# Kernel optimization log

Measured on AMD Instinct MI355X. Metric: run time of the kernel, lower is better.

## Reference

```python
import jax, jax.numpy as jnp
import numpy as np

B, SQ, SKV = 4, 2048, 2048
DQ, DKV, H, NH = 1024, 1024, 1024, 16
HD = H // NH


def setup_inputs() -> dict:
    key = jax.random.key(0)
    ks = jax.random.split(key, 10)
    s = 0.02
    return {
        "query": jax.random.normal(ks[0], (B, SQ, DQ), jnp.float32),
        "key_value": jax.random.normal(ks[1], (B, SKV, DKV), jnp.float32),
        "Wq": jax.random.normal(ks[2], (DQ, H), jnp.float32) * s,
        "bq": jnp.zeros((H,), jnp.float32),
        "Wk": jax.random.normal(ks[3], (DKV, H), jnp.float32) * s,
        "bk": jnp.zeros((H,), jnp.float32),
        "Wv": jax.random.normal(ks[4], (DKV, H), jnp.float32) * s,
        "bv": jnp.zeros((H,), jnp.float32),
        "Wo": jax.random.normal(ks[5], (H, DQ), jnp.float32) * s,
        "bo": jnp.zeros((DQ,), jnp.float32),
    }


def reference(query, key_value, Wq, bq, Wk, bk, Wv, bv, Wo, bo):
    b, sq, _ = query.shape
    skv = key_value.shape[1]
    scale = np.sqrt(HD).astype(np.float32)
    # project and split heads: [B, S, H] -> [B, NH, S, HD]
    q = (query @ Wq + bq).reshape(b, sq, NH, HD).transpose(0, 2, 1, 3)
    k = (key_value @ Wk + bk).reshape(b, skv, NH, HD).transpose(0, 2, 1, 3)
    v = (key_value @ Wv + bv).reshape(b, skv, NH, HD).transpose(0, 2, 1, 3)
    scores = jnp.einsum("bhqd,bhkd->bhqk", q, k) / scale
    attn = jax.nn.softmax(scores, axis=-1)
    out = jnp.einsum("bhqk,bhkd->bhqd", attn, v)
    out = out.transpose(0, 2, 1, 3).reshape(b, sq, NH * HD)
    return out @ Wo + bo
```

## Files before the change

### kernel.cpp

```cpp
#include <hip/hip_runtime.h>


typedef short s16x8 __attribute__((ext_vector_type(8)));
typedef short s16x4 __attribute__((ext_vector_type(4)));
typedef float f32x4 __attribute__((ext_vector_type(4)));
typedef float f32x16 __attribute__((ext_vector_type(16)));
typedef unsigned short u16;
typedef unsigned int u32;

__device__ __forceinline__ u16 f2bf(float f){
    union{float f;u32 u;} v; v.f=f;
    u32 r = v.u + 0x7fffu + ((v.u>>16)&1u);
    return (u16)(r>>16);
}
__device__ __forceinline__ int swz(int row,int colB){ return row*128 + (colB ^ ((row&7)<<4)); }

__device__ __forceinline__ void gl16(const void* g, void* l){
    __builtin_amdgcn_global_load_lds((__attribute__((address_space(1))) void*)(void*)g,
                                     (__attribute__((address_space(3))) void*)l, 16, 0, 0);
}
__device__ __forceinline__ u32 cvtpk(float lo, float hi){
    u32 r; asm("v_cvt_pk_bf16_f32 %0, %1, %2" : "=v"(r) : "v"(lo), "v"(hi)); return r;
}
__device__ __forceinline__ void plswap(u32& a, u32& b){
    asm("v_permlane32_swap_b32 %0, %1" : "+v"(a), "+v"(b));
}

#define QSCALE 0.1803368801111204f

__global__ __launch_bounds__(256) void cvtbf(const float* __restrict__ in, u16* __restrict__ out){
    size_t i = ((size_t)blockIdx.x*256 + threadIdx.x)*8;
    f32x4 a = *(const f32x4*)(in+i), b = *(const f32x4*)(in+i+4);
    s16x8 o;
    #pragma unroll
    for (int j=0;j<4;++j){ o[j]=(short)f2bf(a[j]); o[4+j]=(short)f2bf(b[j]); }
    *(s16x8*)(out+i) = o;
}

__global__ __launch_bounds__(256) void transW(const float* __restrict__ W, u16* __restrict__ Wt){
    __shared__ u16 T[64*68];
    const int tid = threadIdx.x;
    const int n0 = blockIdx.x*64, k0 = blockIdx.y*64;
    const int tr = tid>>4, tc = (tid&15)*4;
    #pragma unroll
    for (int p=0;p<4;++p){
        int k = p*16 + tr;
        f32x4 v = *(const f32x4*)(W + (size_t)(k0+k)*1024 + n0 + tc);
        s16x4 o;
        #pragma unroll
        for (int j=0;j<4;++j) o[j]=(short)f2bf(v[j]);
        *(s16x4*)(T + k*68 + tc) = o;
    }
    __syncthreads();
    #pragma unroll
    for (int p=0;p<4;++p){
        int n = p*16 + tr;
        s16x4 o;
        #pragma unroll
        for (int e=0;e<4;++e) o[e] = (short)T[(tc+e)*68 + n];
        *(s16x4*)(Wt + (size_t)(n0+n)*1024 + k0 + tc) = o;
    }
}

template<int EPI>
__global__ __launch_bounds__(256)
void gemm128(const u16* __restrict__ A, const u16* __restrict__ Bt,
             const float* __restrict__ bias, void* __restrict__ C,
             int M, int N, int K, float scale)
{
    __shared__ __align__(16) u16 As[2][128*64];
    __shared__ __align__(16) u16 Bs[2][128*64];
    const int tid = threadIdx.x, lane = tid&63, wave = tid>>6;
    const int ln = lane&15, g = lane>>4;
    const int wm = wave>>1, wn = wave&1;
    const int bm = blockIdx.x, bn = blockIdx.y;

    f32x4 acc[4][4] = {};

    const int r0g = tid>>3, cc8 = (tid&7)*8;
    const u16* aA = A  + (size_t)(bm*128 + r0g)*K + cc8;
    const u16* aB = Bt + (size_t)(bn*128 + r0g)*K + cc8;

    auto stage = [&](int k0, int buf){
        char* pa = (char*)As[buf] + tid*16;
        char* pb = (char*)Bs[buf] + tid*16;
        #pragma unroll
        for (int i=0;i<4;++i){
            gl16(aA + k0 + i*32*K, pa + i*4096);
            gl16(aB + k0 + i*32*K, pb + i*4096);
        }
    };

    stage(0, 0);
    int cur = 0;
    for (int k0=0; k0<K; k0+=64){
        if (k0+64 < K){
            stage(k0+64, cur^1);
            asm volatile("s_waitcnt vmcnt(8)" ::: "memory");
        } else {
            asm volatile("s_waitcnt vmcnt(0)" ::: "memory");
        }
        __builtin_amdgcn_s_barrier();
        #pragma unroll
        for (int kk=0;kk<2;++kk){
            s16x8 af[4], bf[4];
            #pragma unroll
            for (int mi=0;mi<4;++mi)
                af[mi] = *(const s16x8*)((const char*)As[cur] + (size_t)(wm*64+mi*16+ln)*128 + kk*64 + g*16);
            #pragma unroll
            for (int ni=0;ni<4;++ni)
                bf[ni] = *(const s16x8*)((const char*)Bs[cur] + (size_t)(wn*64+ni*16+ln)*128 + kk*64 + g*16);
            #pragma unroll
            for (int mi=0;mi<4;++mi)
                #pragma unroll
                for (int ni=0;ni<4;++ni)
                    acc[mi][ni] = __builtin_amdgcn_mfma_f32_16x16x32_bf16(af[mi], bf[ni], acc[mi][ni], 0,0,0);
        }
        __builtin_amdgcn_s_barrier();
        cur ^= 1;
    }

    #pragma unroll
    for (int mi=0;mi<4;++mi){
        #pragma unroll
        for (int ni=0;ni<4;++ni){
            int col = bn*128 + wn*64 + ni*16 + ln;
            float bv = bias[col];
            #pragma unroll
            for (int r=0;r<4;++r){
                int row = bm*128 + wm*64 + mi*16 + 4*g + r;
                float v = (acc[mi][ni][r] + bv) * scale;
                if constexpr (EPI==0)
                    ((u16*)C)[(size_t)row*N + col] = f2bf(v);
                else if constexpr (EPI==2){
                    int b = row>>11, s = row&2047;
                    ((u16*)C)[((size_t)(b*1024 + col))*2048 + s] = f2bf(v);
                } else
                    ((float*)C)[(size_t)row*N + col] = v;
            }
        }
    }
}

template<bool A_IS_F32, int EPI>
__global__ __launch_bounds__(256)
void gemm_bias_64(const void* __restrict__ Av, const float* __restrict__ W,
                  const float* __restrict__ bias, void* __restrict__ Cout,
                  int M, int N, int K, float scale)
{
    __shared__ __align__(16) char smem[16384];
    char* As = smem;
    char* Ws = smem + 8192;
    const int tid  = threadIdx.x;
    const int lane = tid & 63, wave = tid >> 6;
    const int g = lane >> 4, ln = lane & 15;
    const int wm = wave >> 1, wn = wave & 1;
    const int bm = blockIdx.x, bn = blockIdx.y;
    f32x4 acc[2][2] = {};
    const int srow = tid >> 2;
    const int sch  = (tid & 3) * 16;

    for (int k0 = 0; k0 < K; k0 += 64) {
        if constexpr (A_IS_F32) {
            const float* a = (const float*)Av + (size_t)(bm*64+srow)*K + k0 + sch;
            const f32x4* a4 = (const f32x4*)a;
            #pragma unroll
            for (int c = 0; c < 2; ++c) {
                f32x4 x = a4[c*2+0], y = a4[c*2+1];
                s16x8 wv;
                #pragma unroll
                for (int j = 0; j < 4; ++j){ wv[j]=(short)f2bf(x[j]); wv[4+j]=(short)f2bf(y[j]); }
                *(s16x8*)(As + swz(srow, sch*2 + c*16)) = wv;
            }
        } else {
            const u16* a = (const u16*)Av + (size_t)(bm*64+srow)*K + k0 + sch;
            *(s16x8*)(As + swz(srow, sch*2 + 0))  = *(const s16x8*)(a + 0);
            *(s16x8*)(As + swz(srow, sch*2 + 16)) = *(const s16x8*)(a + 8);
        }
        {
            const float* wsrc = W + (size_t)(k0+srow)*N + bn*64 + sch;
            #pragma unroll
            for (int j = 0; j < 16; ++j) {
                int n = sch + j;
                *(short*)(Ws + n*128 + ((srow*2) ^ ((n&7)<<4))) = (short)f2bf(wsrc[j]);
            }
        }
        __syncthreads();
        #pragma unroll
        for (int kk = 0; kk < 2; ++kk) {
            s16x8 af[2], bfr[2];
            #pragma unroll
            for (int mi = 0; mi < 2; ++mi)
                af[mi] = *(const s16x8*)(As + swz(wm*32+mi*16+ln, kk*64 + g*16));
            #pragma unroll
            for (int ni = 0; ni < 2; ++ni)
                bfr[ni] = *(const s16x8*)(Ws + swz(wn*32+ni*16+ln, kk*64 + g*16));
            #pragma unroll
            for (int mi = 0; mi < 2; ++mi)
                #pragma unroll
                for (int ni = 0; ni < 2; ++ni)
                    acc[mi][ni] = __builtin_amdgcn_mfma_f32_16x16x32_bf16(af[mi], bfr[ni], acc[mi][ni], 0,0,0);
        }
        __syncthreads();
    }
    #pragma unroll
    for (int mi = 0; mi < 2; ++mi){
        #pragma unroll
        for (int ni = 0; ni < 2; ++ni){
            int col = bn*64 + wn*32 + ni*16 + ln;
            float bv = bias[col];
            #pragma unroll
            for (int r = 0; r < 4; ++r){
                int row = bm*64 + wm*32 + mi*16 + 4*g + r;
                float v = (acc[mi][ni][r] + bv) * scale;
                if constexpr (EPI==0)
                    ((u16*)Cout)[(size_t)row*N + col] = f2bf(v);
                else if constexpr (EPI==2){
                    int b = row>>11, s = row&2047;
                    ((u16*)Cout)[((size_t)(b*1024+col))*2048 + s] = f2bf(v);
                } else
                    ((float*)Cout)[(size_t)row*N + col] = v;
            }
        }
    }
}

__global__ __launch_bounds__(256)
void attn_fwd4(const u16* __restrict__ Q, const u16* __restrict__ K,
               const u16* __restrict__ Vt, u16* __restrict__ O)
{
    __shared__ __align__(16) char smem[32768];
    const int tid = threadIdx.x, lane = tid&63, wave = tid>>6;
    const int l31 = lane&31, hl = lane>>5;

    int dlin = blockIdx.y*16 + blockIdx.x;
    int xc = dlin&7, t = dlin>>3;
    int bh = xc*8 + (t>>4), qt = t&15;
    int b = bh>>4, h = bh&15;

    const int qrow = qt*128 + wave*32 + l31;
    const size_t qgoff = ((size_t)(b*2048 + qrow))*1024 + h*64;
    const u16* Kg = K  + ((size_t)(b*2048))*1024 + h*64;
    const u16* Vg = Vt + ((size_t)(b*1024 + h*64))*2048;

    s16x8 bq[4];
    #pragma unroll
    for (int ks=0;ks<4;++ks)
        bq[ks] = *(const s16x8*)(Q + qgoff + 16*ks + 8*hl);

    float m_run = -1e30f, l_run = 0.0f;
    f32x16 oa0 = {}, oa1 = {};

    const int r0 = tid>>3;
    const int qc = (tid&7) ^ (r0&7);
    const u16* kbase = Kg + (size_t)r0*1024 + qc*8;
    const u16* vbase = Vg + (size_t)r0*2048 + qc*8;
    const int ldst = tid*16;

    auto stage = [&](int kt, int buf){
        char* Kb = smem + buf*16384;
        char* Vb = Kb + 8192;
        const size_t kk = (size_t)kt*65536;
        const int kv0 = kt*64;
        gl16(kbase + kk,           Kb + ldst);
        gl16(kbase + kk + 32768,   Kb + 4096 + ldst);
        gl16(vbase + kv0,          Vb + ldst);
        gl16(vbase + kv0 + 65536,  Vb + 4096 + ldst);
    };

    int kofs[8];
    #pragma unroll
    for (int hk=0;hk<2;++hk)
        #pragma unroll
        for (int ks=0;ks<4;++ks)
            kofs[hk*4+ks] = swz(hk*32 + l31, 32*ks + 16*hl);

    stage(0, 0);
    int cur = 0;

    for (int kt=0; kt<32; ++kt){
        if (kt+1 < 32){
            stage(kt+1, cur^1);
            asm volatile("s_waitcnt vmcnt(4)" ::: "memory");
        } else {
            asm volatile("s_waitcnt vmcnt(0)" ::: "memory");
        }
        __builtin_amdgcn_s_barrier();

        char* Kb = smem + cur*16384;
        char* Vb = Kb + 8192;

        f32x16 s0 = {}, s1 = {};
        __builtin_amdgcn_s_setprio(1);
        #pragma unroll
        for (int ks=0; ks<4; ++ks){
            s16x8 ak0 = *(const s16x8*)(Kb + kofs[ks]);
            s16x8 ak1 = *(const s16x8*)(Kb + kofs[4+ks]);
            s0 = __builtin_amdgcn_mfma_f32_32x32x16_bf16(ak0, bq[ks], s0, 0,0,0);
            s1 = __builtin_amdgcn_mfma_f32_32x32x16_bf16(ak1, bq[ks], s1, 0,0,0);
        }
        __builtin_amdgcn_s_setprio(0);

        float tm[8];
        #pragma unroll
        for (int i=0;i<8;++i) tm[i] = fmaxf(fmaxf(fmaxf(s0[i], s0[i+8]), s1[i]), s1[i+8]);
        float pm = fmaxf(fmaxf(fmaxf(tm[0],tm[1]),fmaxf(tm[2],tm[3])),
                         fmaxf(fmaxf(tm[4],tm[5]),fmaxf(tm[6],tm[7])));
        pm = fmaxf(pm, __shfl_xor(pm, 32));

        if (!__all(pm - m_run <= 8.0f)){
            float mn  = fmaxf(m_run, pm);
            float scl = __builtin_amdgcn_exp2f(m_run - mn);
            oa0 *= scl; oa1 *= scl;
            l_run *= scl;
            m_run = mn;
        }

        #pragma unroll
        for (int r=0; r<16; ++r){
            s0[r] = __builtin_amdgcn_exp2f(s0[r] - m_run);
            s1[r] = __builtin_amdgcn_exp2f(s1[r] - m_run);
        }
        float ts[8];
        #pragma unroll
        for (int i=0;i<8;++i) ts[i] = (s0[i]+s0[i+8]) + (s1[i]+s1[i+8]);
        float rs = ((ts[0]+ts[1])+(ts[2]+ts[3])) + ((ts[4]+ts[5])+(ts[6]+ts[7]));
        rs += __shfl_xor(rs, 32);
        l_run += rs;

        s16x8 bP[4];
        #pragma unroll
        for (int f=0; f<2; ++f){
            const f32x16& sf = f ? s1 : s0;
            u32 W[8];
            #pragma unroll
            for (int w=0; w<8; ++w) W[w] = cvtpk(sf[2*w], sf[2*w+1]);
            #pragma unroll
            for (int s=0; s<2; ++s){
                u32 x0 = W[4*s+0], y0 = W[4*s+2];
                u32 x1 = W[4*s+1], y1 = W[4*s+3];
                plswap(x0, y0);
                plswap(x1, y1);
                union { u32 w[4]; s16x8 v; } u;
                u.w[0]=x0; u.w[1]=x1; u.w[2]=y0; u.w[3]=y1;
                bP[2*f+s] = u.v;
            }
        }

        __builtin_amdgcn_s_setprio(1);
        #pragma unroll
        for (int ks=0; ks<4; ++ks){
            s16x8 av0 = *(const s16x8*)(Vb + kofs[ks]);
            s16x8 av1 = *(const s16x8*)(Vb + kofs[4+ks]);
            oa0 = __builtin_amdgcn_mfma_f32_32x32x16_bf16(av0, bP[ks], oa0, 0,0,0);
            oa1 = __builtin_amdgcn_mfma_f32_32x32x16_bf16(av1, bP[ks], oa1, 0,0,0);
        }
        __builtin_amdgcn_s_setprio(0);

        __builtin_amdgcn_s_barrier();
        cur ^= 1;
    }

    float inv = 1.0f / l_run;
    u16* Ob = O + qgoff;
    #pragma unroll
    for (int fd=0; fd<2; ++fd){
        const f32x16& oaf = fd ? oa1 : oa0;
        #pragma unroll
        for (int rq=0; rq<4; ++rq){
            s16x4 o;
            #pragma unroll
            for (int e=0;e<4;++e) o[e] = (short)f2bf(oaf[rq*4+e] * inv);
            *(s16x4*)(Ob + fd*32 + rq*8 + hl*4) = o;
        }
    }
}

extern "C" void kernel_launch(void* const* d_in, const int* in_sizes, int n_in,
                              void* d_out, int out_size, void* d_ws, size_t ws_size,
                              hipStream_t stream)
{
    const float* query = (const float*)d_in[0];
    const float* kvin  = (const float*)d_in[1];
    const float* Wq = (const float*)d_in[2];
    const float* bq = (const float*)d_in[3];
    const float* Wk = (const float*)d_in[4];
    const float* bk = (const float*)d_in[5];
    const float* Wv = (const float*)d_in[6];
    const float* bv = (const float*)d_in[7];
    const float* Wo = (const float*)d_in[8];
    const float* bo = (const float*)d_in[9];

    const int M = 8192, D = 1024;
    const size_t MB = 1024ull*1024ull;
    u16* Qb  = (u16*)d_ws;
    u16* Kb  = Qb  + 8*MB;
    u16* Vtb = Kb  + 8*MB;
    u16* Ob  = Vtb + 8*MB;

    if (ws_size >= 66*MB) {
        u16* Wt   = Ob + 8*MB;
        u16* qbf  = (u16*)d_out;
        u16* kvbf = qbf + 8*MB;

        cvtbf<<<4096,256,0,stream>>>(query, qbf);
        cvtbf<<<4096,256,0,stream>>>(kvin,  kvbf);

        dim3 tg(16,16), gg(64,8);
        transW<<<tg,256,0,stream>>>(Wq, Wt);
        gemm128<0><<<gg,256,0,stream>>>(qbf,  Wt, bq, Qb,  M, D, D, QSCALE);
        transW<<<tg,256,0,stream>>>(Wk, Wt);
        gemm128<0><<<gg,256,0,stream>>>(kvbf, Wt, bk, Kb,  M, D, D, 1.0f);
        transW<<<tg,256,0,stream>>>(Wv, Wt);
        gemm128<2><<<gg,256,0,stream>>>(kvbf, Wt, bv, Vtb, M, D, D, 1.0f);

        attn_fwd4<<<dim3(16,64),256,0,stream>>>(Qb, Kb, Vtb, Ob);

        transW<<<tg,256,0,stream>>>(Wo, Wt);
        gemm128<3><<<gg,256,0,stream>>>(Ob, Wt, bo, d_out, M, D, D, 1.0f);
    } else {
        dim3 gg(128,16);
        gemm_bias_64<true ,0><<<gg,256,0,stream>>>(query, Wq, bq, Qb,  M, D, D, QSCALE);
        gemm_bias_64<true ,0><<<gg,256,0,stream>>>(kvin,  Wk, bk, Kb,  M, D, D, 1.0f);
        gemm_bias_64<true ,2><<<gg,256,0,stream>>>(kvin,  Wv, bv, Vtb, M, D, D, 1.0f);
        attn_fwd4<<<dim3(16,64),256,0,stream>>>(Qb, Kb, Vtb, Ob);
        gemm_bias_64<false,3><<<gg,256,0,stream>>>(Ob, Wo, bo, d_out, M, D, D, 1.0f);
    }
}
```

Before: 235.5 us.

## Software-pipeline QK^T ahead of softmax/PV in attention and batch prep launches

The attention loop is restructured so that the QK^T MFMAs for the next KV tile are issued before the softmax and PV of the current tile. Staging runs two tiles ahead so matrix work can overlap the exp/pack VALU work and the global loads. Separately, the two fp32-to-bf16 conversions are merged into one launch and the three projection-weight transposes into one 3D-grid launch, with Wo transposed later into a reused buffer. This trades higher register pressure from the extra live score tile for fewer launches and better MFMA/VALU overlap.

```diff
diff --git a/kernel.cpp b/kernel.cpp
--- a/kernel.cpp
+++ b/kernel.cpp
@@ -28,16 +28,20 @@
 
 #define QSCALE 0.1803368801111204f
 
-__global__ __launch_bounds__(256) void cvtbf(const float* __restrict__ in, u16* __restrict__ out){
-    size_t i = ((size_t)blockIdx.x*256 + threadIdx.x)*8;
-    f32x4 a = *(const f32x4*)(in+i), b = *(const f32x4*)(in+i+4);
+__global__ __launch_bounds__(256) void cvtbf2(const float* __restrict__ a, const float* __restrict__ b,
+                                              u16* __restrict__ oa, u16* __restrict__ ob){
+    int blk = blockIdx.x;
+    const float* in = a; u16* out = oa;
+    if (blk >= 4096){ in = b; out = ob; blk -= 4096; }
+    size_t i = ((size_t)blk*256 + threadIdx.x)*8;
+    f32x4 x = *(const f32x4*)(in+i), y = *(const f32x4*)(in+i+4);
     s16x8 o;
     #pragma unroll
-    for (int j=0;j<4;++j){ o[j]=(short)f2bf(a[j]); o[4+j]=(short)f2bf(b[j]); }
+    for (int j=0;j<4;++j){ o[j]=(short)f2bf(x[j]); o[4+j]=(short)f2bf(y[j]); }
     *(s16x8*)(out+i) = o;
 }
 
-__global__ __launch_bounds__(256) void transW(const float* __restrict__ W, u16* __restrict__ Wt){
+__device__ __forceinline__ void transW_body(const float* __restrict__ W, u16* __restrict__ Wt){
     __shared__ u16 T[64*68];
     const int tid = threadIdx.x;
     const int n0 = blockIdx.x*64, k0 = blockIdx.y*64;
@@ -60,6 +64,16 @@
         for (int e=0;e<4;++e) o[e] = (short)T[(tc+e)*68 + n];
         *(s16x4*)(Wt + (size_t)(n0+n)*1024 + k0 + tc) = o;
     }
+}
+__global__ __launch_bounds__(256) void transW(const float* __restrict__ W, u16* __restrict__ Wt){
+    transW_body(W, Wt);
+}
+__global__ __launch_bounds__(256) void transW3(const float* __restrict__ W0, const float* __restrict__ W1,
+                                               const float* __restrict__ W2,
+                                               u16* __restrict__ O0, u16* __restrict__ O1, u16* __restrict__ O2){
+    const float* W = blockIdx.z==0 ? W0 : (blockIdx.z==1 ? W1 : W2);
+    u16*       Wt = blockIdx.z==0 ? O0 : (blockIdx.z==1 ? O1 : O2);
+    transW_body(W, Wt);
 }
 
 template<int EPI>
@@ -226,7 +240,7 @@
 }
 
 __global__ __launch_bounds__(256)
-void attn_fwd4(const u16* __restrict__ Q, const u16* __restrict__ K,
+void attn_fwd5(const u16* __restrict__ Q, const u16* __restrict__ K,
                const u16* __restrict__ Vt, u16* __restrict__ O)
 {
     __shared__ __align__(16) char smem[32768];
@@ -234,8 +248,8 @@
     const int l31 = lane&31, hl = lane>>5;
 
     int dlin = blockIdx.y*16 + blockIdx.x;
-    int xc = dlin&7, t = dlin>>3;
-    int bh = xc*8 + (t>>4), qt = t&15;
+    int xc = dlin&7, t0 = dlin>>3;
+    int bh = xc*8 + (t0>>4), qt = t0&15;
     int b = bh>>4, h = bh&15;
 
     const int qrow = qt*128 + wave*32 + l31;
@@ -260,12 +274,12 @@
     auto stage = [&](int kt, int buf){
         char* Kb = smem + buf*16384;
         char* Vb = Kb + 8192;
-        const size_t kk = (size_t)kt*65536;
+        const size_t kkOff = (size_t)kt*65536;
         const int kv0 = kt*64;
-        gl16(kbase + kk,           Kb + ldst);
-        gl16(kbase + kk + 32768,   Kb + 4096 + ldst);
-        gl16(vbase + kv0,          Vb + ldst);
-        gl16(vbase + kv0 + 65536,  Vb + 4096 + ldst);
+        gl16(kbase + kkOff,           Kb + ldst);
+        gl16(kbase + kkOff + 32768,   Kb + 4096 + ldst);
+        gl16(vbase + kv0,             Vb + ldst);
+        gl16(vbase + kv0 + 65536,     Vb + 4096 + ldst);
     };
 
     int kofs[8];
@@ -275,39 +289,28 @@
         for (int ks=0;ks<4;++ks)
             kofs[hk*4+ks] = swz(hk*32 + l31, 32*ks + 16*hl);
 
-    stage(0, 0);
-    int cur = 0;
-
-    for (int kt=0; kt<32; ++kt){
-        if (kt+1 < 32){
-            stage(kt+1, cur^1);
-            asm volatile("s_waitcnt vmcnt(4)" ::: "memory");
-        } else {
-            asm volatile("s_waitcnt vmcnt(0)" ::: "memory");
-        }
-        __builtin_amdgcn_s_barrier();
-
-        char* Kb = smem + cur*16384;
-        char* Vb = Kb + 8192;
-
-        f32x16 s0 = {}, s1 = {};
+    auto qk = [&](int buf, f32x16& sA, f32x16& sB){
+        char* Kb = smem + buf*16384;
+        f32x16 a = {}, c = {};
         __builtin_amdgcn_s_setprio(1);
         #pragma unroll
         for (int ks=0; ks<4; ++ks){
             s16x8 ak0 = *(const s16x8*)(Kb + kofs[ks]);
             s16x8 ak1 = *(const s16x8*)(Kb + kofs[4+ks]);
-            s0 = __builtin_amdgcn_mfma_f32_32x32x16_bf16(ak0, bq[ks], s0, 0,0,0);
-            s1 = __builtin_amdgcn_mfma_f32_32x32x16_bf16(ak1, bq[ks], s1, 0,0,0);
+            a = __builtin_amdgcn_mfma_f32_32x32x16_bf16(ak0, bq[ks], a, 0,0,0);
+            c = __builtin_amdgcn_mfma_f32_32x32x16_bf16(ak1, bq[ks], c, 0,0,0);
         }
         __builtin_amdgcn_s_setprio(0);
-
+        sA = a; sB = c;
+    };
+
+    auto smpack = [&](f32x16& s0, f32x16& s1, s16x8* bP){
         float tm[8];
         #pragma unroll
         for (int i=0;i<8;++i) tm[i] = fmaxf(fmaxf(fmaxf(s0[i], s0[i+8]), s1[i]), s1[i+8]);
         float pm = fmaxf(fmaxf(fmaxf(tm[0],tm[1]),fmaxf(tm[2],tm[3])),
                          fmaxf(fmaxf(tm[4],tm[5]),fmaxf(tm[6],tm[7])));
         pm = fmaxf(pm, __shfl_xor(pm, 32));
-
         if (!__all(pm - m_run <= 8.0f)){
             float mn  = fmaxf(m_run, pm);
             float scl = __builtin_amdgcn_exp2f(m_run - mn);
@@ -315,7 +318,6 @@
             l_run *= scl;
             m_run = mn;
         }
-
         #pragma unroll
         for (int r=0; r<16; ++r){
             s0[r] = __builtin_amdgcn_exp2f(s0[r] - m_run);
@@ -327,8 +329,6 @@
         float rs = ((ts[0]+ts[1])+(ts[2]+ts[3])) + ((ts[4]+ts[5])+(ts[6]+ts[7]));
         rs += __shfl_xor(rs, 32);
         l_run += rs;
-
-        s16x8 bP[4];
         #pragma unroll
         for (int f=0; f<2; ++f){
             const f32x16& sf = f ? s1 : s0;
@@ -346,7 +346,10 @@
                 bP[2*f+s] = u.v;
             }
         }
-
+    };
+
+    auto pv = [&](int buf, const s16x8* bP){
+        char* Vb = smem + buf*16384 + 8192;
         __builtin_amdgcn_s_setprio(1);
         #pragma unroll
         for (int ks=0; ks<4; ++ks){
@@ -356,9 +359,42 @@
             oa1 = __builtin_amdgcn_mfma_f32_32x32x16_bf16(av1, bP[ks], oa1, 0,0,0);
         }
         __builtin_amdgcn_s_setprio(0);
-
+    };
+
+    int cur = 0;
+    auto body = [&](f32x16& sC0, f32x16& sC1, f32x16& sN0, f32x16& sN1, int kt){
+        asm volatile("s_waitcnt vmcnt(2)" ::: "memory");
         __builtin_amdgcn_s_barrier();
+        qk(cur^1, sN0, sN1);
+        s16x8 bP[4];
+        smpack(sC0, sC1, bP);
+        pv(cur, bP);
+        __builtin_amdgcn_s_barrier();
+        if (kt < 30) stage(kt+2, cur);
         cur ^= 1;
+    };
+
+    stage(0, 0);
+    stage(1, 1);
+    asm volatile("s_waitcnt vmcnt(6)" ::: "memory");
+    __builtin_amdgcn_s_barrier();
+    f32x16 sa, sb, sc, sd;
+    qk(0, sa, sb);
+
+    int kt = 0;
+    #pragma unroll 1
+    for (int it=0; it<15; ++it){
+        body(sa, sb, sc, sd, kt); ++kt;
+        body(sc, sd, sa, sb, kt); ++kt;
+    }
+    body(sa, sb, sc, sd, kt); ++kt;
+
+    asm volatile("s_waitcnt vmcnt(0)" ::: "memory");
+    __builtin_amdgcn_s_barrier();
+    {
+        s16x8 bP[4];
+        smpack(sc, sd, bP);
+        pv(cur, bP);
     }
 
     float inv = 1.0f / l_run;
@@ -399,31 +435,30 @@
     u16* Ob  = Vtb + 8*MB;
 
     if (ws_size >= 66*MB) {
-        u16* Wt   = Ob + 8*MB;
+        u16* Wt0  = Ob + 8*MB;
+        u16* Wt1  = Ob;
+        u16* Wt2  = Ob + 1*MB;
         u16* qbf  = (u16*)d_out;
         u16* kvbf = qbf + 8*MB;
 
-        cvtbf<<<4096,256,0,stream>>>(query, qbf);
-        cvtbf<<<4096,256,0,stream>>>(kvin,  kvbf);
-
-        dim3 tg(16,16), gg(64,8);
-        transW<<<tg,256,0,stream>>>(Wq, Wt);
-        gemm128<0><<<gg,256,0,stream>>>(qbf,  Wt, bq, Qb,  M, D, D, QSCALE);
-        transW<<<tg,256,0,stream>>>(Wk, Wt);
-        gemm128<0><<<gg,256,0,stream>>>(kvbf, Wt, bk, Kb,  M, D, D, 1.0f);
-        transW<<<tg,256,0,stream>>>(Wv, Wt);
-        gemm128<2><<<gg,256,0,stream>>>(kvbf, Wt, bv, Vtb, M, D, D, 1.0f);
-
-        attn_fwd4<<<dim3(16,64),256,0,stream>>>(Qb, Kb, Vtb, Ob);
-
-        transW<<<tg,256,0,stream>>>(Wo, Wt);
-        gemm128<3><<<gg,256,0,stream>>>(Ob, Wt, bo, d_out, M, D, D, 1.0f);
+        cvtbf2<<<8192,256,0,stream>>>(query, kvin, qbf, kvbf);
+
+        dim3 tg3(16,16,3), tg(16,16), gg(64,8);
+        transW3<<<tg3,256,0,stream>>>(Wq, Wk, Wv, Wt0, Wt1, Wt2);
+        gemm128<0><<<gg,256,0,stream>>>(qbf,  Wt0, bq, Qb,  M, D, D, QSCALE);
+        transW<<<tg,256,0,stream>>>(Wo, Wt0);
+        gemm128<0><<<gg,256,0,stream>>>(kvbf, Wt1, bk, Kb,  M, D, D, 1.0f);
+        gemm128<2><<<gg,256,0,stream>>>(kvbf, Wt2, bv, Vtb, M, D, D, 1.0f);
+
+        attn_fwd5<<<dim3(16,64),256,0,stream>>>(Qb, Kb, Vtb, Ob);
+
+        gemm128<3><<<gg,256,0,stream>>>(Ob, Wt0, bo, d_out, M, D, D, 1.0f);
     } else {
         dim3 gg(128,16);
         gemm_bias_64<true ,0><<<gg,256,0,stream>>>(query, Wq, bq, Qb,  M, D, D, QSCALE);
         gemm_bias_64<true ,0><<<gg,256,0,stream>>>(kvin,  Wk, bk, Kb,  M, D, D, 1.0f);
         gemm_bias_64<true ,2><<<gg,256,0,stream>>>(kvin,  Wv, bv, Vtb, M, D, D, 1.0f);
-        attn_fwd4<<<dim3(16,64),256,0,stream>>>(Qb, Kb, Vtb, Ob);
+        attn_fwd5<<<dim3(16,64),256,0,stream>>>(Qb, Kb, Vtb, Ob);
         gemm_bias_64<false,3><<<gg,256,0,stream>>>(Ob, Wo, bo, d_out, M, D, D, 1.0f);
     }
 }
```

Result: faster. 230.3 us (-2.2%).
